# Performance work log

Hardware: AMD Instinct MI355X
Metric: run time of the kernel (lower is better)

The kernel has to match this reference:

```python
import jax, jax.numpy as jnp
import numpy as np

VOCAB, EMBED, HIDDEN, BATCH, SEQ = 32000, 512, 1024, 64, 512


def _xavier(key, shape):
    fan_out, fan_in = shape
    limit = float(np.sqrt(6.0 / (fan_in + fan_out)))
    return jax.random.uniform(key, shape, jnp.float32, -limit, limit)


def setup_inputs() -> dict:
    key = jax.random.key(0)
    ks = jax.random.split(key, 12)
    inp = {
        "texts": jax.random.randint(ks[0], (BATCH, SEQ), 0, VOCAB, dtype=jnp.int32),
        "emb": jax.random.normal(ks[1], (VOCAB, EMBED), jnp.float32),
        # layer 0: input_dim = EMBED
        "Wf0": _xavier(ks[2], (HIDDEN, EMBED + HIDDEN)), "bf0": jnp.zeros((HIDDEN,), jnp.float32),
        "Wi0": _xavier(ks[3], (HIDDEN, EMBED + HIDDEN)), "bi0": jnp.zeros((HIDDEN,), jnp.float32),
        "Wo0": _xavier(ks[4], (HIDDEN, EMBED + HIDDEN)), "bo0": jnp.zeros((HIDDEN,), jnp.float32),
        "Wc0": _xavier(ks[5], (HIDDEN, EMBED + HIDDEN)), "bc0": jnp.zeros((HIDDEN,), jnp.float32),
        # layer 1: input_dim = HIDDEN
        "Wf1": _xavier(ks[6], (HIDDEN, 2 * HIDDEN)), "bf1": jnp.zeros((HIDDEN,), jnp.float32),
        "Wi1": _xavier(ks[7], (HIDDEN, 2 * HIDDEN)), "bi1": jnp.zeros((HIDDEN,), jnp.float32),
        "Wo1": _xavier(ks[8], (HIDDEN, 2 * HIDDEN)), "bo1": jnp.zeros((HIDDEN,), jnp.float32),
        "Wc1": _xavier(ks[9], (HIDDEN, 2 * HIDDEN)), "bc1": jnp.zeros((HIDDEN,), jnp.float32),
        "Wy": _xavier(ks[10], (VOCAB, HIDDEN)), "by": jnp.zeros((VOCAB,), jnp.float32),
    }
    return inp


def _lstm_layer(xs, Wf, bf, Wi, bi, Wo, bo, Wc, bc):
    # xs: (T, B, F). torch.cat((h, x), dim=0) -> weight cols are [h | x].
    B = xs.shape[1]
    H = Wf.shape[0]
    h0 = jnp.zeros((B, H), xs.dtype)
    c0 = jnp.zeros((B, H), xs.dtype)

    def step(carry, x):
        h, c = carry
        concat = jnp.concatenate([h, x], axis=1)  # (B, H+F)
        ft = jax.nn.sigmoid(concat @ Wf.T + bf)
        it = jax.nn.sigmoid(concat @ Wi.T + bi)
        c_hat = jnp.tanh(concat @ Wc.T + bc)
        c = ft * c + it * c_hat
        ot = jax.nn.sigmoid(concat @ Wo.T + bo)
        h = ot * jnp.tanh(c)
        return (h, c), h

    (_, _), hs = jax.lax.scan(step, (h0, c0), xs)
    return hs  # (T, B, H)


def reference(texts, emb, Wf0, bf0, Wi0, bi0, Wo0, bo0, Wc0, bc0,
              Wf1, bf1, Wi1, bi1, Wo1, bo1, Wc1, bc1, Wy, by):
    # embedded: (T, B, E)
    xs = jnp.transpose(emb[texts], (1, 0, 2))
    hs0 = _lstm_layer(xs, Wf0, bf0, Wi0, bi0, Wo0, bo0, Wc0, bc0)
    hs1 = _lstm_layer(hs0, Wf1, bf1, Wi1, bi1, Wo1, bo1, Wc1, bc1)
    h_last = hs1[-1]  # (B, H) = last timestep of last layer (finetune=True branch)
    y = h_last @ Wy.T + by  # (B, VOCAB); .squeeze(1) in torch is a no-op for VOCAB>1
    return y
```

## Files before the change

### kernel.cpp

```cpp
#include <hip/hip_runtime.h>
#include <stdint.h>
#include <stddef.h>

#define T_SEQ  512
#define NBATCH 64
#define EMBED  512
#define HIDDEN 1024
#define VOCAB  32000
#define NWG    128
#define NTHR   256
#define AGENT  __HIP_MEMORY_SCOPE_AGENT
#define RING   260
#define SLOT_E (NBATCH * 2048)
#define BOUND  250

#define RST   66
#define PBUF  (64 * RST)

#define FLG(cnt, l, t)  ((cnt) + ((((t) << 1) | (l)) << 5))
#define AGG1(cnt, t)    ((cnt) + ((1024 + (t)) << 5))
#define INITC(cnt)      ((cnt) + (1540 << 5))

typedef __attribute__((ext_vector_type(8))) short short8;
typedef __attribute__((ext_vector_type(4))) float f32x4;

__device__ __forceinline__ unsigned short f2bf(float x) {
  union { float f; unsigned u; } v; v.f = x;
  unsigned r = v.u + 0x7FFFu + ((v.u >> 16) & 1u);
  return (unsigned short)(r >> 16);
}
__device__ __forceinline__ float sigm(float x) { return 1.0f / (1.0f + __expf(-x)); }
__device__ __forceinline__ float tanh_(float x) {
  float e = __expf(2.0f * x);
  return 1.0f - 2.0f / (e + 1.0f);
}

__device__ __forceinline__ unsigned ld_flag(unsigned* p) {
  return __hip_atomic_load(p, __ATOMIC_RELAXED, AGENT);
}
__device__ __forceinline__ void wait_flag(unsigned* p, unsigned tgt) {
  while (__hip_atomic_load(p, __ATOMIC_RELAXED, AGENT) < tgt)
    __builtin_amdgcn_s_sleep(2);
}

__global__ void embed_k(const int* __restrict__ texts, const float* __restrict__ emb,
                        unsigned short* __restrict__ xs) {
  const int bid = blockIdx.x;
  const int t = bid >> 6, b = bid & 63;
  const int row = texts[b * T_SEQ + t];
  const float* src = emb + (size_t)row * EMBED;
  const int e = threadIdx.x * 2;
  float2 v = *(const float2*)(src + e);
  unsigned pk = (unsigned)f2bf(v.x) | ((unsigned)f2bf(v.y) << 16);
  *(unsigned*)(xs + (size_t)bid * EMBED + e) = pk;
}

template<int LAYER>
__device__ __forceinline__ void run_layer(
    const unsigned short* __restrict__ xs_all,
    unsigned short* __restrict__ state,
    unsigned* __restrict__ cnt,
    const float* __restrict__ W0, const float* __restrict__ W1,
    const float* __restrict__ W2, const float* __restrict__ W3,
    const float* __restrict__ B0, const float* __restrict__ B1,
    const float* __restrict__ B2, const float* __restrict__ B3,
    float* buf, int w, int tid)
{
  constexpr int K  = LAYER ? 2048 : 1536;
  constexpr int KT = K / 128;
  const int lane = tid & 63;
  const int wid  = tid >> 6;
  const int ln   = lane & 15;
  const int qq   = lane >> 4;
  const int d0   = (tid & 7) * 2;
  const int bp   = (tid >> 3) * 2;
  const int gk0  = w * 16 + d0;

  short8 wreg[KT][4];
  const float* Wg[4] = {W0, W1, W2, W3};
  #pragma unroll
  for (int mt = 0; mt < 4; ++mt) {
    const float* row = Wg[mt] + (size_t)(w * 16 + ln) * K;
    #pragma unroll
    for (int kt = 0; kt < KT; ++kt) {
      int col;
      if (LAYER == 1) col = wid * 512 + kt * 32;
      else col = (kt < 4) ? (1024 + wid * 128 + kt * 32) : (wid * 256 + (kt - 4) * 32);
      col += qq * 8;
      f32x4 lo = *(const f32x4*)(row + col);
      f32x4 hi = *(const f32x4*)(row + col + 4);
      short8 v;
      v[0] = (short)f2bf(lo[0]); v[1] = (short)f2bf(lo[1]);
      v[2] = (short)f2bf(lo[2]); v[3] = (short)f2bf(lo[3]);
      v[4] = (short)f2bf(hi[0]); v[5] = (short)f2bf(hi[1]);
      v[6] = (short)f2bf(hi[2]); v[7] = (short)f2bf(hi[3]);
      wreg[kt][mt] = v;
    }
  }

  float bs[4][2];
  #pragma unroll
  for (int g = 0; g < 4; ++g) {
    const float* Bg = (g == 0) ? B0 : (g == 1) ? B1 : (g == 2) ? B2 : B3;
    bs[g][0] = Bg[gk0]; bs[g][1] = Bg[gk0 + 1];
  }
  float cst[2][2] = {{0.f, 0.f}, {0.f, 0.f}};

  wait_flag(INITC(cnt), NWG);
  asm volatile("" ::: "memory");

  for (int t = 0; t < T_SEQ; ++t) {
    const int so  = t % RING;
    const int so1 = (t + 1) % RING;
    const unsigned short* slotT  = state + (size_t)so  * SLOT_E;
    const unsigned short* slotT1 = state + (size_t)so1 * SLOT_E;
    f32x4 acc[4][4] = {};

    unsigned war = 64;
    if (LAYER == 0 && t >= BOUND) war = ld_flag(AGG1(cnt, t - BOUND));

    if constexpr (LAYER == 0) {
      unsigned* flp = FLG(cnt, 0, (t > 0) ? t - 1 : 0) + 2 * wid;
      unsigned fv[2] = {8u, 8u};
      if (t > 0) { fv[0] = ld_flag(flp); fv[1] = ld_flag(flp + 1); }

      const unsigned short* xrow = xs_all + (size_t)t * (NBATCH * EMBED);
      #pragma unroll
      for (int kt = 0; kt < 4; ++kt) {
        const int bc = wid * 128 + kt * 32 + qq * 8;
        short8 bf[4];
        #pragma unroll
        for (int nt = 0; nt < 4; ++nt)
          bf[nt] = *(const short8*)(xrow + (size_t)(nt * 16 + ln) * EMBED + bc);
        #pragma unroll
        for (int mt = 0; mt < 4; ++mt)
          #pragma unroll
          for (int nt = 0; nt < 4; ++nt)
            acc[mt][nt] = __builtin_amdgcn_mfma_f32_16x16x32_bf16(
                wreg[kt][mt], bf[nt], acc[mt][nt], 0, 0, 0);
      }
      const unsigned short* hbase = slotT + 1024;
      #pragma unroll
      for (int c = 0; c < 2; ++c) {
        if (t > 0 && fv[c] < 8u) wait_flag(flp + c, 8u);
        asm volatile("" ::: "memory");
        #pragma unroll
        for (int k2 = 0; k2 < 4; ++k2) {
          const int kt = 4 + c * 4 + k2;
          const int hc = wid * 256 + c * 128 + k2 * 32 + qq * 8;
          short8 bf[4];
          #pragma unroll
          for (int nt = 0; nt < 4; ++nt)
            bf[nt] = *(const short8*)(hbase + (size_t)(nt * 16 + ln) * 2048 + hc);
          #pragma unroll
          for (int mt = 0; mt < 4; ++mt)
            #pragma unroll
            for (int nt = 0; nt < 4; ++nt)
              acc[mt][nt] = __builtin_amdgcn_mfma_f32_16x16x32_bf16(
                  wreg[kt][mt], bf[nt], acc[mt][nt], 0, 0, 0);
        }
      }
    } else {
      unsigned* flp = (wid < 2) ? FLG(cnt, 1, (t > 0) ? t - 1 : 0) + 4 * wid
                                : FLG(cnt, 0, t) + 4 * (wid - 2);
      const bool need = (wid >= 2) || (t > 0);
      unsigned fv[4] = {8u, 8u, 8u, 8u};
      if (need) {
        fv[0] = ld_flag(flp);     fv[1] = ld_flag(flp + 1);
        fv[2] = ld_flag(flp + 2); fv[3] = ld_flag(flp + 3);
      }
      const unsigned short* base = (wid < 2) ? slotT : slotT1;
      #pragma unroll
      for (int c = 0; c < 4; ++c) {
        if (need && fv[c] < 8u) wait_flag(flp + c, 8u);
        asm volatile("" ::: "memory");
        #pragma unroll
        for (int k2 = 0; k2 < 4; ++k2) {
          const int kt = c * 4 + k2;
          const int cc = wid * 512 + c * 128 + k2 * 32 + qq * 8;
          short8 bf[4];
          #pragma unroll
          for (int nt = 0; nt < 4; ++nt)
            bf[nt] = *(const short8*)(base + (size_t)(nt * 16 + ln) * 2048 + cc);
          #pragma unroll
          for (int mt = 0; mt < 4; ++mt)
            #pragma unroll
            for (int nt = 0; nt < 4; ++nt)
              acc[mt][nt] = __builtin_amdgcn_mfma_f32_16x16x32_bf16(
                  wreg[kt][mt], bf[nt], acc[mt][nt], 0, 0, 0);
        }
      }
    }

    {
      float* bb = buf + wid * PBUF;
      #pragma unroll
      for (int mt = 0; mt < 4; ++mt)
        #pragma unroll
        for (int nt = 0; nt < 4; ++nt)
          #pragma unroll
          for (int j = 0; j < 4; ++j)
            bb[(mt * 16 + qq * 4 + j) * RST + nt * 16 + ln] = acc[mt][nt][j];
    }
    __syncthreads();

    float gv[4][2][2];
    #pragma unroll
    for (int gt = 0; gt < 4; ++gt)
      #pragma unroll
      for (int dd = 0; dd < 2; ++dd) {
        float sx = bs[gt][dd], sy = bs[gt][dd];
        #pragma unroll
        for (int p = 0; p < 4; ++p) {
          float2 v = *(const float2*)&buf[p * PBUF + (gt * 16 + d0 + dd) * RST + bp];
          sx += v.x; sy += v.y;
        }
        gv[gt][dd][0] = sx; gv[gt][dd][1] = sy;
      }

    if (LAYER == 0 && t >= BOUND && war < 64)
      wait_flag(AGG1(cnt, t - BOUND), 64);

    unsigned* su = (unsigned*)state;
    const size_t obase = (size_t)so1 * SLOT_E + (LAYER == 0 ? 1024 : 0) + gk0;
    #pragma unroll
    for (int s2 = 0; s2 < 2; ++s2) {
      cst[0][s2] = sigm(gv[0][0][s2]) * cst[0][s2] + sigm(gv[1][0][s2]) * tanh_(gv[3][0][s2]);
      cst[1][s2] = sigm(gv[0][1][s2]) * cst[1][s2] + sigm(gv[1][1][s2]) * tanh_(gv[3][1][s2]);
      const float h0v = sigm(gv[2][0][s2]) * tanh_(cst[0][s2]);
      const float h1v = sigm(gv[2][1][s2]) * tanh_(cst[1][s2]);
      const unsigned pk = (unsigned)f2bf(h0v) | ((unsigned)f2bf(h1v) << 16);
      __hip_atomic_store(su + ((obase + (size_t)(bp + s2) * 2048) >> 1), pk,
                         __ATOMIC_RELAXED, AGENT);
    }
    __syncthreads();
    if (tid == 0) {
      __hip_atomic_fetch_add(FLG(cnt, LAYER, t) + (w >> 3), 1u,
                             __ATOMIC_RELAXED, AGENT);
      if (LAYER == 1)
        __hip_atomic_fetch_add(AGG1(cnt, t), 1u, __ATOMIC_RELAXED, AGENT);
    }
  }
}

__launch_bounds__(NTHR, 1)
__global__ void lstm_k(const unsigned short* __restrict__ xs,
                       unsigned short* __restrict__ state,
                       unsigned* __restrict__ cnt,
                       const float* __restrict__ Wf0, const float* __restrict__ Wi0,
                       const float* __restrict__ Wo0, const float* __restrict__ Wc0,
                       const float* __restrict__ bf0, const float* __restrict__ bi0,
                       const float* __restrict__ bo0, const float* __restrict__ bc0,
                       const float* __restrict__ Wf1, const float* __restrict__ Wi1,
                       const float* __restrict__ Wo1, const float* __restrict__ Wc1,
                       const float* __restrict__ bf1, const float* __restrict__ bi1,
                       const float* __restrict__ bo1, const float* __restrict__ bc1)
{
  __shared__ __align__(16) float buf[4 * PBUF];
  const int tid = threadIdx.x;
  const int gw  = blockIdx.x;

  {
    unsigned* su = (unsigned*)state;
    const int idx = gw * NTHR + tid;
    __hip_atomic_store(su + idx,         0u, __ATOMIC_RELAXED, AGENT);
    __hip_atomic_store(su + 32768 + idx, 0u, __ATOMIC_RELAXED, AGENT);
    __syncthreads();
    if (tid == 0)
      __hip_atomic_fetch_add(INITC(cnt), 1u, __ATOMIC_RELAXED, AGENT);
  }

  if (gw < 64)
    run_layer<0>(xs, state, cnt, Wf0, Wi0, Wo0, Wc0, bf0, bi0, bo0, bc0,
                 buf, gw, tid);
  else
    run_layer<1>(nullptr, state, cnt, Wf1, Wi1, Wo1, Wc1, bf1, bi1, bo1, bc1,
                 buf, gw - 64, tid);
}

__global__ void final_k(const float* __restrict__ Wy,
                        const unsigned short* __restrict__ hlast,
                        const float* __restrict__ by,
                        float* __restrict__ out)
{
  const int tid = threadIdx.x, lane = tid & 63, wid = tid >> 6;
  const int ln = lane & 15, qq = lane >> 4;
  const int vbase = (blockIdx.x * 4 + wid) * 16;
  f32x4 acc[4] = {};
  const float* arow = Wy + (size_t)(vbase + ln) * HIDDEN;
  for (int kt = 0; kt < 32; ++kt) {
    const int kk = kt * 32 + qq * 8;
    f32x4 lo = *(const f32x4*)(arow + kk);
    f32x4 hi = *(const f32x4*)(arow + kk + 4);
    short8 a;
    a[0] = (short)f2bf(lo[0]); a[1] = (short)f2bf(lo[1]);
    a[2] = (short)f2bf(lo[2]); a[3] = (short)f2bf(lo[3]);
    a[4] = (short)f2bf(hi[0]); a[5] = (short)f2bf(hi[1]);
    a[6] = (short)f2bf(hi[2]); a[7] = (short)f2bf(hi[3]);
    #pragma unroll
    for (int nt = 0; nt < 4; ++nt) {
      short8 bv = *(const short8*)(hlast + (size_t)(nt * 16 + ln) * 2048 + kk);
      acc[nt] = __builtin_amdgcn_mfma_f32_16x16x32_bf16(a, bv, acc[nt], 0, 0, 0);
    }
  }
  const int v0 = vbase + qq * 4;
  const f32x4 bias = *(const f32x4*)(by + v0);
  #pragma unroll
  for (int nt = 0; nt < 4; ++nt) {
    const int bb = nt * 16 + ln;
    f32x4 r = acc[nt] + bias;
    *(f32x4*)(out + (size_t)bb * VOCAB + v0) = r;
  }
}

extern "C" void kernel_launch(void* const* d_in, const int* in_sizes, int n_in,
                              void* d_out, int out_size, void* d_ws, size_t ws_size,
                              hipStream_t stream) {
  (void)in_sizes; (void)n_in; (void)out_size; (void)ws_size;
  const int*   texts = (const int*)d_in[0];
  const float* emb   = (const float*)d_in[1];
  const float* Wf0 = (const float*)d_in[2];  const float* bf0 = (const float*)d_in[3];
  const float* Wi0 = (const float*)d_in[4];  const float* bi0 = (const float*)d_in[5];
  const float* Wo0 = (const float*)d_in[6];  const float* bo0 = (const float*)d_in[7];
  const float* Wc0 = (const float*)d_in[8];  const float* bc0 = (const float*)d_in[9];
  const float* Wf1 = (const float*)d_in[10]; const float* bf1 = (const float*)d_in[11];
  const float* Wi1 = (const float*)d_in[12]; const float* bi1 = (const float*)d_in[13];
  const float* Wo1 = (const float*)d_in[14]; const float* bo1 = (const float*)d_in[15];
  const float* Wc1 = (const float*)d_in[16]; const float* bc1 = (const float*)d_in[17];
  const float* Wy  = (const float*)d_in[18]; const float* by  = (const float*)d_in[19];

  char* ws = (char*)d_ws;
  unsigned*       cnt   = (unsigned*)ws;
  unsigned short* state = (unsigned short*)(ws + 262144);
  unsigned short* xs    = (unsigned short*)(ws + 262144 + (size_t)RING * SLOT_E * 2);
  float* out = (float*)d_out;

  hipMemsetAsync(cnt, 0, 262144, stream);
  embed_k<<<T_SEQ * NBATCH, 256, 0, stream>>>(texts, emb, xs);
  lstm_k<<<NWG, NTHR, 0, stream>>>(xs, state, cnt,
                                   Wf0, Wi0, Wo0, Wc0, bf0, bi0, bo0, bc0,
                                   Wf1, Wi1, Wo1, Wc1, bf1, bi1, bo1, bc1);
  final_k<<<VOCAB / 64, 256, 0, stream>>>(
      Wy, state + (size_t)(T_SEQ % RING) * SLOT_E, by, out);
}
```

Baseline: 5.776 ms.

## Co-locate both LSTM layers in each workgroup with per-half LDS barriers

Each workgroup now runs 512 threads: one 256-thread half handles 8 hidden units of layer 0 and the other half handles 8 units of layer 1. This replaces the old split of 64 workgroups per layer with 16 units each. The halves synchronise through LDS atomic counters with spin-waits rather than __syncthreads, so the two layers' recurrences can proceed independently inside the same workgroup. Per-step work per wave is halved and flag targets rise to 16 per group. The aim is to spread both layers across all 128 workgroups and cut barrier cost, at the price of spin-wait overhead, more VGPR pressure per CU, and a subtler memory-ordering scheme.

```diff
diff --git a/kernel.cpp b/kernel.cpp
--- a/kernel.cpp
+++ b/kernel.cpp
@@ -8,14 +8,15 @@
 #define HIDDEN 1024
 #define VOCAB  32000
 #define NWG    128
-#define NTHR   256
+#define NTHR   512
 #define AGENT  __HIP_MEMORY_SCOPE_AGENT
+#define WGSCOPE __HIP_MEMORY_SCOPE_WORKGROUP
 #define RING   260
 #define SLOT_E (NBATCH * 2048)
 #define BOUND  250
 
 #define RST   66
-#define PBUF  (64 * RST)
+#define PB    (32 * RST)
 
 #define FLG(cnt, l, t)  ((cnt) + ((((t) << 1) | (l)) << 5))
 #define AGG1(cnt, t)    ((cnt) + ((1024 + (t)) << 5))
@@ -40,7 +41,16 @@
 }
 __device__ __forceinline__ void wait_flag(unsigned* p, unsigned tgt) {
   while (__hip_atomic_load(p, __ATOMIC_RELAXED, AGENT) < tgt)
-    __builtin_amdgcn_s_sleep(2);
+    __builtin_amdgcn_s_sleep(1);
+  asm volatile("" ::: "memory");
+}
+__device__ __forceinline__ void lds_add(unsigned* p) {
+  __hip_atomic_fetch_add(p, 1u, __ATOMIC_RELAXED, WGSCOPE);
+}
+__device__ __forceinline__ void lds_wait(unsigned* p, unsigned tgt) {
+  while (__hip_atomic_load(p, __ATOMIC_RELAXED, WGSCOPE) < tgt)
+    __builtin_amdgcn_s_sleep(1);
+  asm volatile("" ::: "memory");
 }
 
 __global__ void embed_k(const int* __restrict__ texts, const float* __restrict__ emb,
@@ -56,7 +66,7 @@
 }
 
 template<int LAYER>
-__device__ __forceinline__ void run_layer(
+__device__ __forceinline__ void run_half(
     const unsigned short* __restrict__ xs_all,
     unsigned short* __restrict__ state,
     unsigned* __restrict__ cnt,
@@ -64,28 +74,30 @@
     const float* __restrict__ W2, const float* __restrict__ W3,
     const float* __restrict__ B0, const float* __restrict__ B1,
     const float* __restrict__ B2, const float* __restrict__ B3,
-    float* buf, int w, int tid)
+    float* bufh, unsigned* lc, int w, int th)
 {
   constexpr int K  = LAYER ? 2048 : 1536;
   constexpr int KT = K / 128;
-  const int lane = tid & 63;
-  const int wid  = tid >> 6;
+  const int lane = th & 63;
+  const int wv   = th >> 6;
   const int ln   = lane & 15;
   const int qq   = lane >> 4;
-  const int d0   = (tid & 7) * 2;
-  const int bp   = (tid >> 3) * 2;
-  const int gk0  = w * 16 + d0;
-
-  short8 wreg[KT][4];
+  const int d0   = (th & 3) * 2;
+  const int b    = th >> 2;
+  const int gk0  = w * 8 + d0;
+  const bool w0  = (lane == 0);
+
+  short8 wreg[KT][2];
   const float* Wg[4] = {W0, W1, W2, W3};
   #pragma unroll
-  for (int mt = 0; mt < 4; ++mt) {
-    const float* row = Wg[mt] + (size_t)(w * 16 + ln) * K;
+  for (int mt = 0; mt < 2; ++mt) {
+    const int r = mt * 16 + ln;
+    const float* row = Wg[r >> 3] + (size_t)(w * 8 + (r & 7)) * K;
     #pragma unroll
     for (int kt = 0; kt < KT; ++kt) {
       int col;
-      if (LAYER == 1) col = wid * 512 + kt * 32;
-      else col = (kt < 4) ? (1024 + wid * 128 + kt * 32) : (wid * 256 + (kt - 4) * 32);
+      if (LAYER == 1) col = wv * 512 + kt * 32;
+      else col = (kt < 4) ? (1024 + wv * 128 + kt * 32) : (wv * 256 + (kt - 4) * 32);
       col += qq * 8;
       f32x4 lo = *(const f32x4*)(row + col);
       f32x4 hi = *(const f32x4*)(row + col + 4);
@@ -97,43 +109,42 @@
       wreg[kt][mt] = v;
     }
   }
-
   float bs[4][2];
   #pragma unroll
   for (int g = 0; g < 4; ++g) {
     const float* Bg = (g == 0) ? B0 : (g == 1) ? B1 : (g == 2) ? B2 : B3;
     bs[g][0] = Bg[gk0]; bs[g][1] = Bg[gk0 + 1];
   }
-  float cst[2][2] = {{0.f, 0.f}, {0.f, 0.f}};
+  float c0 = 0.0f, c1 = 0.0f;
 
   wait_flag(INITC(cnt), NWG);
-  asm volatile("" ::: "memory");
 
   for (int t = 0; t < T_SEQ; ++t) {
     const int so  = t % RING;
     const int so1 = (t + 1) % RING;
     const unsigned short* slotT  = state + (size_t)so  * SLOT_E;
     const unsigned short* slotT1 = state + (size_t)so1 * SLOT_E;
-    f32x4 acc[4][4] = {};
-
-    unsigned war = 64;
+
+    lds_wait(lc + 2, 4u * t);
+
+    unsigned war = 0xFFFFFFFFu;
     if (LAYER == 0 && t >= BOUND) war = ld_flag(AGG1(cnt, t - BOUND));
 
+    f32x4 acc[2][4] = {};
     if constexpr (LAYER == 0) {
-      unsigned* flp = FLG(cnt, 0, (t > 0) ? t - 1 : 0) + 2 * wid;
-      unsigned fv[2] = {8u, 8u};
+      unsigned* flp = FLG(cnt, 0, (t > 0) ? t - 1 : 0) + 2 * wv;
+      unsigned fv[2] = {16u, 16u};
       if (t > 0) { fv[0] = ld_flag(flp); fv[1] = ld_flag(flp + 1); }
-
       const unsigned short* xrow = xs_all + (size_t)t * (NBATCH * EMBED);
       #pragma unroll
       for (int kt = 0; kt < 4; ++kt) {
-        const int bc = wid * 128 + kt * 32 + qq * 8;
+        const int bc = wv * 128 + kt * 32 + qq * 8;
         short8 bf[4];
         #pragma unroll
         for (int nt = 0; nt < 4; ++nt)
           bf[nt] = *(const short8*)(xrow + (size_t)(nt * 16 + ln) * EMBED + bc);
         #pragma unroll
-        for (int mt = 0; mt < 4; ++mt)
+        for (int mt = 0; mt < 2; ++mt)
           #pragma unroll
           for (int nt = 0; nt < 4; ++nt)
             acc[mt][nt] = __builtin_amdgcn_mfma_f32_16x16x32_bf16(
@@ -142,18 +153,18 @@
       const unsigned short* hbase = slotT + 1024;
       #pragma unroll
       for (int c = 0; c < 2; ++c) {
-        if (t > 0 && fv[c] < 8u) wait_flag(flp + c, 8u);
+        if (t > 0 && fv[c] < 16u) wait_flag(flp + c, 16u);
         asm volatile("" ::: "memory");
         #pragma unroll
         for (int k2 = 0; k2 < 4; ++k2) {
           const int kt = 4 + c * 4 + k2;
-          const int hc = wid * 256 + c * 128 + k2 * 32 + qq * 8;
+          const int hc = wv * 256 + c * 128 + k2 * 32 + qq * 8;
           short8 bf[4];
           #pragma unroll
           for (int nt = 0; nt < 4; ++nt)
             bf[nt] = *(const short8*)(hbase + (size_t)(nt * 16 + ln) * 2048 + hc);
           #pragma unroll
-          for (int mt = 0; mt < 4; ++mt)
+          for (int mt = 0; mt < 2; ++mt)
             #pragma unroll
             for (int nt = 0; nt < 4; ++nt)
               acc[mt][nt] = __builtin_amdgcn_mfma_f32_16x16x32_bf16(
@@ -161,29 +172,30 @@
         }
       }
     } else {
-      unsigned* flp = (wid < 2) ? FLG(cnt, 1, (t > 0) ? t - 1 : 0) + 4 * wid
-                                : FLG(cnt, 0, t) + 4 * (wid - 2);
-      const bool need = (wid >= 2) || (t > 0);
-      unsigned fv[4] = {8u, 8u, 8u, 8u};
+      unsigned* flp = (wv < 2) ? FLG(cnt, 1, (t > 0) ? t - 1 : 0) + 4 * wv
+                               : FLG(cnt, 0, t) + 4 * (wv - 2);
+      const bool need = (wv >= 2) || (t > 0);
+      unsigned fv[4] = {16u, 16u, 16u, 16u};
       if (need) {
         fv[0] = ld_flag(flp);     fv[1] = ld_flag(flp + 1);
         fv[2] = ld_flag(flp + 2); fv[3] = ld_flag(flp + 3);
       }
-      const unsigned short* base = (wid < 2) ? slotT : slotT1;
+      const unsigned short* base = (wv < 2) ? slotT : (slotT1 + 1024);
+      const int coff = (wv < 2) ? wv * 512 : (wv - 2) * 512;
       #pragma unroll
       for (int c = 0; c < 4; ++c) {
-        if (need && fv[c] < 8u) wait_flag(flp + c, 8u);
+        if (need && fv[c] < 16u) wait_flag(flp + c, 16u);
         asm volatile("" ::: "memory");
         #pragma unroll
         for (int k2 = 0; k2 < 4; ++k2) {
           const int kt = c * 4 + k2;
-          const int cc = wid * 512 + c * 128 + k2 * 32 + qq * 8;
+          const int cc = coff + c * 128 + k2 * 32 + qq * 8;
           short8 bf[4];
           #pragma unroll
           for (int nt = 0; nt < 4; ++nt)
             bf[nt] = *(const short8*)(base + (size_t)(nt * 16 + ln) * 2048 + cc);
           #pragma unroll
-          for (int mt = 0; mt < 4; ++mt)
+          for (int mt = 0; mt < 2; ++mt)
             #pragma unroll
             for (int nt = 0; nt < 4; ++nt)
               acc[mt][nt] = __builtin_amdgcn_mfma_f32_16x16x32_bf16(
@@ -193,49 +205,50 @@
     }
 
     {
-      float* bb = buf + wid * PBUF;
-      #pragma unroll
-      for (int mt = 0; mt < 4; ++mt)
+      float* bb = bufh + wv * PB;
+      #pragma unroll
+      for (int mt = 0; mt < 2; ++mt)
         #pragma unroll
         for (int nt = 0; nt < 4; ++nt)
           #pragma unroll
           for (int j = 0; j < 4; ++j)
             bb[(mt * 16 + qq * 4 + j) * RST + nt * 16 + ln] = acc[mt][nt][j];
     }
-    __syncthreads();
-
-    float gv[4][2][2];
+    asm volatile("s_waitcnt lgkmcnt(0)" ::: "memory");
+    if (w0) lds_add(lc + 0);
+    lds_wait(lc + 0, 4u * (t + 1));
+
+    float gv[4][2];
     #pragma unroll
     for (int gt = 0; gt < 4; ++gt)
       #pragma unroll
       for (int dd = 0; dd < 2; ++dd) {
-        float sx = bs[gt][dd], sy = bs[gt][dd];
-        #pragma unroll
-        for (int p = 0; p < 4; ++p) {
-          float2 v = *(const float2*)&buf[p * PBUF + (gt * 16 + d0 + dd) * RST + bp];
-          sx += v.x; sy += v.y;
-        }
-        gv[gt][dd][0] = sx; gv[gt][dd][1] = sy;
-      }
-
-    if (LAYER == 0 && t >= BOUND && war < 64)
-      wait_flag(AGG1(cnt, t - BOUND), 64);
-
-    unsigned* su = (unsigned*)state;
-    const size_t obase = (size_t)so1 * SLOT_E + (LAYER == 0 ? 1024 : 0) + gk0;
-    #pragma unroll
-    for (int s2 = 0; s2 < 2; ++s2) {
-      cst[0][s2] = sigm(gv[0][0][s2]) * cst[0][s2] + sigm(gv[1][0][s2]) * tanh_(gv[3][0][s2]);
-      cst[1][s2] = sigm(gv[0][1][s2]) * cst[1][s2] + sigm(gv[1][1][s2]) * tanh_(gv[3][1][s2]);
-      const float h0v = sigm(gv[2][0][s2]) * tanh_(cst[0][s2]);
-      const float h1v = sigm(gv[2][1][s2]) * tanh_(cst[1][s2]);
-      const unsigned pk = (unsigned)f2bf(h0v) | ((unsigned)f2bf(h1v) << 16);
-      __hip_atomic_store(su + ((obase + (size_t)(bp + s2) * 2048) >> 1), pk,
-                         __ATOMIC_RELAXED, AGENT);
-    }
-    __syncthreads();
-    if (tid == 0) {
-      __hip_atomic_fetch_add(FLG(cnt, LAYER, t) + (w >> 3), 1u,
+        float s = bs[gt][dd];
+        #pragma unroll
+        for (int p = 0; p < 4; ++p)
+          s += bufh[p * PB + (gt * 8 + d0 + dd) * RST + b];
+        gv[gt][dd] = s;
+      }
+    asm volatile("s_waitcnt lgkmcnt(0)" ::: "memory");
+    if (w0) lds_add(lc + 2);
+
+    if (LAYER == 0 && t >= BOUND && war < 128u)
+      wait_flag(AGG1(cnt, t - BOUND), 128u);
+
+    c0 = sigm(gv[0][0]) * c0 + sigm(gv[1][0]) * tanh_(gv[3][0]);
+    c1 = sigm(gv[0][1]) * c1 + sigm(gv[1][1]) * tanh_(gv[3][1]);
+    const float h0v = sigm(gv[2][0]) * tanh_(c0);
+    const float h1v = sigm(gv[2][1]) * tanh_(c1);
+    const unsigned pk = (unsigned)f2bf(h0v) | ((unsigned)f2bf(h1v) << 16);
+    const size_t oe = (size_t)so1 * SLOT_E + (size_t)b * 2048
+                    + (LAYER == 0 ? 1024 : 0) + gk0;
+    __hip_atomic_store((unsigned*)state + (oe >> 1), pk, __ATOMIC_RELAXED, AGENT);
+
+    asm volatile("s_waitcnt vmcnt(0)" ::: "memory");
+    if (w0) lds_add(lc + 1);
+    if (th == 0) {
+      lds_wait(lc + 1, 4u * (t + 1));
+      __hip_atomic_fetch_add(FLG(cnt, LAYER, t) + (w >> 4), 1u,
                              __ATOMIC_RELAXED, AGENT);
       if (LAYER == 1)
         __hip_atomic_fetch_add(AGG1(cnt, t), 1u, __ATOMIC_RELAXED, AGENT);
@@ -243,7 +256,7 @@
   }
 }
 
-__launch_bounds__(NTHR, 1)
+__launch_bounds__(NTHR, 2)
 __global__ void lstm_k(const unsigned short* __restrict__ xs,
                        unsigned short* __restrict__ state,
                        unsigned* __restrict__ cnt,
@@ -256,26 +269,26 @@
                        const float* __restrict__ bf1, const float* __restrict__ bi1,
                        const float* __restrict__ bo1, const float* __restrict__ bc1)
 {
-  __shared__ __align__(16) float buf[4 * PBUF];
+  __shared__ __align__(16) float buf[8 * PB];
+  __shared__ unsigned lc[2][8];
   const int tid = threadIdx.x;
   const int gw  = blockIdx.x;
 
+  if (tid < 16) ((unsigned*)lc)[tid] = 0u;
   {
     unsigned* su = (unsigned*)state;
-    const int idx = gw * NTHR + tid;
-    __hip_atomic_store(su + idx,         0u, __ATOMIC_RELAXED, AGENT);
-    __hip_atomic_store(su + 32768 + idx, 0u, __ATOMIC_RELAXED, AGENT);
-    __syncthreads();
-    if (tid == 0)
-      __hip_atomic_fetch_add(INITC(cnt), 1u, __ATOMIC_RELAXED, AGENT);
-  }
-
-  if (gw < 64)
-    run_layer<0>(xs, state, cnt, Wf0, Wi0, Wo0, Wc0, bf0, bi0, bo0, bc0,
-                 buf, gw, tid);
+    __hip_atomic_store(su + gw * NTHR + tid, 0u, __ATOMIC_RELAXED, AGENT);
+  }
+  __syncthreads();
+  if (tid == 0)
+    __hip_atomic_fetch_add(INITC(cnt), 1u, __ATOMIC_RELAXED, AGENT);
+
+  if (tid < 256)
+    run_half<0>(xs, state, cnt, Wf0, Wi0, Wo0, Wc0, bf0, bi0, bo0, bc0,
+                buf, lc[0], gw, tid);
   else
-    run_layer<1>(nullptr, state, cnt, Wf1, Wi1, Wo1, Wc1, bf1, bi1, bo1, bc1,
-                 buf, gw - 64, tid);
+    run_half<1>(nullptr, state, cnt, Wf1, Wi1, Wo1, Wc1, bf1, bi1, bo1, bc1,
+                buf + 4 * PB, lc[1], gw, tid - 256);
 }
 
 __global__ void final_k(const float* __restrict__ Wy,
```

New measurement: 12.16 ms. 111% more time.
